# Optimization experiments

Measured on AMD Instinct MI355X. Metric: run time of the kernel, lower is better.

## Reference

```python
import jax, jax.numpy as jnp
import numpy as np

DIM = 3456      # visual_dim
E = 1024        # embed_dim = dim_head*heads = 128*8
H = 8
D = E // H
LN_EPS = 1e-5


def _mlp(x, w1, b1, w2, b2):
    # nn.Sequential(Linear, GELU(exact), Linear)
    h = jax.nn.gelu(x @ w1.T + b1, approximate=False)
    return h @ w2.T + b2


def _ln(x, g, b):
    m = jnp.mean(x, axis=-1, keepdims=True)
    v = jnp.mean((x - m) ** 2, axis=-1, keepdims=True)
    return (x - m) * jax.lax.rsqrt(v + LN_EPS) * g + b


def setup_inputs() -> dict:
    key = jax.random.key(0)
    ks = jax.random.split(key, 24)
    std = 0.02
    d = {"x": jax.random.normal(ks[0], (5, 729, DIM), dtype=jnp.float32)}
    i = 1
    for name in ("q", "k", "v"):
        d[f"{name}_w1"] = std * jax.random.normal(ks[i], (E, DIM), dtype=jnp.float32); i += 1
        d[f"{name}_b1"] = jnp.zeros((E,), jnp.float32)
        d[f"{name}_w2"] = std * jax.random.normal(ks[i], (E, E), dtype=jnp.float32); i += 1
        d[f"{name}_b2"] = jnp.zeros((E,), jnp.float32)
        d[f"ln_{name}_g"] = jnp.ones((E,), jnp.float32)
        d[f"ln_{name}_b"] = jnp.zeros((E,), jnp.float32)
    d["in_proj_w"] = std * jax.random.normal(ks[i], (3 * E, E), dtype=jnp.float32); i += 1
    d["in_proj_b"] = jnp.zeros((3 * E,), jnp.float32)
    d["out_proj_w"] = std * jax.random.normal(ks[i], (E, E), dtype=jnp.float32); i += 1
    d["out_proj_b"] = jnp.zeros((E,), jnp.float32)
    d["to_out_w"] = std * jax.random.normal(ks[i], (DIM, E), dtype=jnp.float32)
    return d


def reference(x,
              q_w1, q_b1, q_w2, q_b2, ln_q_g, ln_q_b,
              k_w1, k_b1, k_w2, k_b2, ln_k_g, ln_k_b,
              v_w1, v_b1, v_w2, v_b2, ln_v_g, ln_v_b,
              in_proj_w, in_proj_b, out_proj_w, out_proj_b, to_out_w):
    t, hw, c = x.shape
    # spatial_temporal pattern: x_multi = x, no interpolation.
    # q/k/v: MLP -> LN -> permute(1,0,2) -> divide_feature -> flatten.
    # divide_feature is a pure permutation of tokens; all tokens end up in a
    # single (L, 1, E) attention, so full attention over the flattened
    # (hw, t) token order computes the identical result.
    q = _ln(_mlp(x, q_w1, q_b1, q_w2, q_b2), ln_q_g, ln_q_b)  # (t, hw, E)
    k = _ln(_mlp(x, k_w1, k_b1, k_w2, k_b2), ln_k_g, ln_k_b)
    v = _ln(_mlp(x, v_w1, v_b1, v_w2, v_b2), ln_v_g, ln_v_b)
    L = t * hw
    q = q.transpose(1, 0, 2).reshape(L, E)  # (hw*t, E), (h,w,t)-major order
    k = k.transpose(1, 0, 2).reshape(L, E)
    v = v.transpose(1, 0, 2).reshape(L, E)
    # nn.MultiheadAttention with packed in_proj
    qp = (q @ in_proj_w[:E].T + in_proj_b[:E]).reshape(L, H, D)
    kp = (k @ in_proj_w[E:2 * E].T + in_proj_b[E:2 * E]).reshape(L, H, D)
    vp = (v @ in_proj_w[2 * E:].T + in_proj_b[2 * E:]).reshape(L, H, D)
    scale = 1.0 / jnp.sqrt(jnp.asarray(D, q.dtype))
    scores = jnp.einsum('qhd,khd->hqk', qp, kp) * scale  # (H, L, L)
    attn = jax.nn.softmax(scores, axis=-1)
    o = jnp.einsum('hqk,khd->qhd', attn, vp).reshape(L, E)
    o = o @ out_proj_w.T + out_proj_b
    o = o.reshape(hw, t, E).transpose(1, 0, 2)  # (t, hw, E)
    out = o @ to_out_w.T                         # (t, hw, c)
    return x + out
```

## Files before the change

kernel.cpp:

```cpp
#include <hip/hip_runtime.h>
#include <hip/hip_bf16.h>

#define L_TOK 3645
#define MP    3712
#define DIMV  3456
#define EDIM  1024

typedef __attribute__((ext_vector_type(8))) short bf8;
typedef __attribute__((ext_vector_type(4))) short s4v;
typedef __attribute__((ext_vector_type(4))) float f4;

__device__ __forceinline__ short f2b(float f) {
  union { float f; unsigned u; } v; v.f = f;
  unsigned r = v.u + 0x7fffu + ((v.u >> 16) & 1u);
  return (short)(r >> 16);
}
__device__ __forceinline__ float b2f(short s) {
  union { unsigned u; float f; } v; v.u = ((unsigned)(unsigned short)s) << 16;
  return v.f;
}
__device__ __forceinline__ void gld16(const void* g, void* l) {
  __builtin_amdgcn_global_load_lds(
      (const __attribute__((address_space(1))) void*)(unsigned long long)g,
      (__attribute__((address_space(3))) void*)(unsigned)(unsigned long long)l,
      16, 0, 0);
}

__global__ __launch_bounds__(256) void k_cvt(const float* __restrict__ src,
                                             short* __restrict__ dst, int n4) {
  int i = blockIdx.x * 256 + threadIdx.x;
  if (i >= n4) return;
  float4 v = ((const float4*)src)[i];
  s4v o; o[0] = f2b(v.x); o[1] = f2b(v.y); o[2] = f2b(v.z); o[3] = f2b(v.w);
  ((s4v*)dst)[i] = o;
}
__global__ __launch_bounds__(256) void k_cvt_pad(const float* __restrict__ src,
                                                 short* __restrict__ dst, int n4src, int n4tot) {
  int i = blockIdx.x * 256 + threadIdx.x;
  if (i >= n4tot) return;
  s4v o; o[0] = 0; o[1] = 0; o[2] = 0; o[3] = 0;
  if (i < n4src) {
    float4 v = ((const float4*)src)[i];
    o[0] = f2b(v.x); o[1] = f2b(v.y); o[2] = f2b(v.z); o[3] = f2b(v.w);
  }
  ((s4v*)dst)[i] = o;
}

#define GM_GELU   0
#define GM_BIAS   1
#define GM_QSCALE 2
#define GM_RESID  3

template<int MODE>
__global__ __launch_bounds__(256)
void k_gemm(const short* __restrict__ A, long sA,
            const short* __restrict__ B, long sB,
            const float* __restrict__ bias0, const float* __restrict__ bias1,
            const float* __restrict__ bias2,
            void* __restrict__ Cout, long sC,
            int N, int K, const float* __restrict__ resid)
{
  __shared__ short As[3][128 * 32];
  __shared__ short Bs[3][128 * 32];
  const int tid  = threadIdx.x;
  const int z    = blockIdx.z;

  const int nwg  = gridDim.x * gridDim.y;
  const int orig = blockIdx.y * gridDim.x + blockIdx.x;
  const int qq   = nwg >> 3, rr = nwg & 7;
  const int xcd  = orig & 7, ofs = orig >> 3;
  const int swz  = (xcd < rr ? xcd * (qq + 1) : rr * (qq + 1) + (xcd - rr) * qq) + ofs;
  const int brow = (swz / gridDim.x) * 128;
  const int bcol = (swz % gridDim.x) * 128;

  const short* Ab = A + (long)z * sA;
  const short* Bb = B + (long)z * sB;
  const float* bias = (z == 0) ? bias0 : (z == 1 ? bias1 : bias2);

  const int wave = tid >> 6, lane = tid & 63;
  const int lg = lane >> 4, lc = lane & 15;
  const int m0 = (wave >> 1) * 64, n0 = (wave & 1) * 64;

  const int r0 = tid >> 2, seg = tid & 3;
  const int r1 = r0 + 64;
  const int so0 = (seg ^ ((r0 >> 1) & 3)) * 8;
  const int so1 = (seg ^ ((r1 >> 1) & 3)) * 8;
  const short* pA0 = Ab + (long)(brow + r0) * K + so0;
  const short* pA1 = Ab + (long)(brow + r1) * K + so1;
  const short* pB0 = Bb + (long)(bcol + r0) * K + so0;
  const short* pB1 = Bb + (long)(bcol + r1) * K + so1;

  f4 acc[4][4];
  f4 zero = {0.f, 0.f, 0.f, 0.f};
#pragma unroll
  for (int i = 0; i < 4; ++i)
#pragma unroll
    for (int j = 0; j < 4; ++j) acc[i][j] = zero;

  auto STAGE = [&](int buf) {
    gld16(pA0, &As[buf][tid * 8]);
    gld16(pA1, &As[buf][(tid + 256) * 8]);
    gld16(pB0, &Bs[buf][tid * 8]);
    gld16(pB1, &Bs[buf][(tid + 256) * 8]);
    pA0 += 32; pA1 += 32; pB0 += 32; pB1 += 32;
  };

  const int NT = K >> 5;
  STAGE(0);
  STAGE(1);

  for (int t = 0; t < NT; ++t) {
    const int buf = t % 3;
    if (t < NT - 1) { asm volatile("s_waitcnt vmcnt(4)" ::: "memory"); }
    else           { asm volatile("s_waitcnt vmcnt(0)" ::: "memory"); }
    __builtin_amdgcn_sched_barrier(0);
    __builtin_amdgcn_s_barrier();
    if (t + 2 < NT) STAGE((t + 2) % 3);

    const short* Al = &As[buf][0];
    const short* Bl = &Bs[buf][0];
    bf8 af[4], bfr[4];
#pragma unroll
    for (int mi = 0; mi < 4; ++mi) {
      int r = m0 + mi * 16 + lc;
      af[mi] = *(const bf8*)&Al[r * 32 + ((lg ^ ((r >> 1) & 3)) * 8)];
    }
#pragma unroll
    for (int ni = 0; ni < 4; ++ni) {
      int r = n0 + ni * 16 + lc;
      bfr[ni] = *(const bf8*)&Bl[r * 32 + ((lg ^ ((r >> 1) & 3)) * 8)];
    }
#pragma unroll
    for (int mi = 0; mi < 4; ++mi)
#pragma unroll
      for (int ni = 0; ni < 4; ++ni)
        acc[mi][ni] = __builtin_amdgcn_mfma_f32_16x16x32_bf16(af[mi], bfr[ni], acc[mi][ni], 0, 0, 0);
    __builtin_amdgcn_sched_barrier(0);
  }

  if (MODE == GM_RESID) {
    float* C = (float*)Cout;
#pragma unroll
    for (int ni = 0; ni < 4; ++ni) {
      int col = bcol + n0 + ni * 16 + lc;
#pragma unroll
      for (int mi = 0; mi < 4; ++mi)
#pragma unroll
        for (int r = 0; r < 4; ++r) {
          int row = brow + m0 + mi * 16 + lg * 4 + r;
          if (row < L_TOK)
            C[(long)row * N + col] = acc[mi][ni][r] + resid[(long)row * N + col];
        }
    }
  } else {
    short* C = (short*)Cout + (long)z * sC;
    const float alpha = (MODE == GM_QSCALE && z == 0) ? 0.08838834764831845f : 1.0f;
#pragma unroll
    for (int ni = 0; ni < 4; ++ni) {
      int col = bcol + n0 + ni * 16 + lc;
      float bv = bias[col];
#pragma unroll
      for (int mi = 0; mi < 4; ++mi)
#pragma unroll
        for (int r = 0; r < 4; ++r) {
          int row = brow + m0 + mi * 16 + lg * 4 + r;
          float v = acc[mi][ni][r] + bv;
          if (MODE == GM_GELU) v = 0.5f * v * (1.f + erff(v * 0.70710678118654752f));
          v *= alpha;
          C[(long)row * EDIM + col] = f2b(v);
        }
    }
  }
}

__global__ __launch_bounds__(256)
void k_ln(const short* __restrict__ A, short* __restrict__ Y,
          const float* __restrict__ g0, const float* __restrict__ g1, const float* __restrict__ g2,
          const float* __restrict__ b0, const float* __restrict__ b1, const float* __restrict__ b2)
{
  const int row = blockIdx.x, z = blockIdx.y;
  const float* g = (z == 0) ? g0 : (z == 1 ? g1 : g2);
  const float* b = (z == 0) ? b0 : (z == 1 ? b1 : b2);
  const short* a = A + ((long)z * MP + row) * EDIM;
  short* y = Y + ((long)z * MP + row) * EDIM;
  const int t = threadIdx.x;
  s4v v = *(const s4v*)&a[t * 4];
  float x0 = b2f(v[0]), x1 = b2f(v[1]), x2 = b2f(v[2]), x3 = b2f(v[3]);
  float s = x0 + x1 + x2 + x3;
  float q = x0 * x0 + x1 * x1 + x2 * x2 + x3 * x3;
#pragma unroll
  for (int off = 1; off < 64; off <<= 1) { s += __shfl_xor(s, off); q += __shfl_xor(q, off); }
  __shared__ float rs[4], rq[4];
  if ((t & 63) == 0) { rs[t >> 6] = s; rq[t >> 6] = q; }
  __syncthreads();
  s = rs[0] + rs[1] + rs[2] + rs[3];
  q = rq[0] + rq[1] + rq[2] + rq[3];
  float mean = s * (1.f / 1024.f);
  float var  = q * (1.f / 1024.f) - mean * mean;
  float rstd = rsqrtf(var + 1e-5f);
  s4v o;
#pragma unroll
  for (int j = 0; j < 4; ++j) {
    int col = t * 4 + j;
    o[j] = f2b((b2f(v[j]) - mean) * rstd * g[col] + b[col]);
  }
  *(s4v*)&y[t * 4] = o;
}

__global__ __launch_bounds__(256)
void k_vtrans(const short* __restrict__ vp, short* __restrict__ vpT)
{
  const int kb = blockIdx.x * 64, h = blockIdx.y;
  __shared__ short T[64 * 128];
  const int tid = threadIdx.x;
#pragma unroll
  for (int i = 0; i < 4; ++i) {
    int c = tid + 256 * i;
    int r = c >> 4, x = c & 15;
    bf8 val = *(const bf8*)&vp[(long)(kb + r) * EDIM + h * 128 + x * 8];
    *(bf8*)&T[r * 128 + ((x ^ (r & 7)) * 8)] = val;
  }
  __syncthreads();
#pragma unroll
  for (int i = 0; i < 4; ++i) {
    int c = tid + 256 * i;
    int dr = c >> 3, x = c & 7;
    short tmp[8];
#pragma unroll
    for (int e = 0; e < 8; ++e) {
      int kv = x * 8 + e;
      tmp[e] = T[kv * 128 + (((dr >> 3) ^ (kv & 7)) << 3) + (dr & 7)];
    }
    *(bf8*)&vpT[((long)h * 128 + dr) * MP + kb + x * 8] = *(bf8*)tmp;
  }
}

__global__ __launch_bounds__(256)
void k_attn(const short* __restrict__ qp, const short* __restrict__ kp,
            const short* __restrict__ vpT, short* __restrict__ o)
{
  const int bx = blockIdx.x;
  const int h = bx & 7, qb = (bx >> 3) * 64;
  const int tid = threadIdx.x, wave = tid >> 6, lane = tid & 63;
  const int lg = lane >> 4, lc = lane & 15;
  __shared__ short Ks[64 * 128];
  __shared__ short Vs[128 * 64];
  __shared__ short Ps[4][16 * 64];

  const int qrow = qb + wave * 16 + lc;
  bf8 qf[4];
#pragma unroll
  for (int d4 = 0; d4 < 4; ++d4)
    qf[d4] = *(const bf8*)&qp[(long)qrow * EDIM + h * 128 + d4 * 32 + lg * 8];

  f4 oacc[8];
  f4 zero = {0.f, 0.f, 0.f, 0.f};
#pragma unroll
  for (int dt = 0; dt < 8; ++dt) oacc[dt] = zero;
  float lsum = 0.f;

  for (int kb = 0; kb < L_TOK; kb += 64) {
#pragma unroll
    for (int i = 0; i < 4; ++i) {
      int c = tid + 256 * i; int r = c >> 4, x = c & 15;
      gld16(&kp[(long)(kb + r) * EDIM + h * 128 + (x ^ (r & 7)) * 8], &Ks[c * 8]);
    }
#pragma unroll
    for (int i = 0; i < 4; ++i) {
      int c = tid + 256 * i; int dr = c >> 3, x = c & 7;
      gld16(&vpT[((long)h * 128 + dr) * MP + kb + (x ^ (dr & 7)) * 8], &Vs[c * 8]);
    }
    __syncthreads();

#pragma unroll
    for (int s = 0; s < 4; ++s) {
      f4 sa = zero;
      const int krow = s * 16 + lc;
#pragma unroll
      for (int d4 = 0; d4 < 4; ++d4) {
        bf8 kf = *(const bf8*)&Ks[krow * 128 + (((d4 * 4 + lg) ^ (krow & 7)) * 8)];
        sa = __builtin_amdgcn_mfma_f32_16x16x32_bf16(kf, qf[d4], sa, 0, 0, 0);
      }
      const int kvb = kb + s * 16 + lg * 4;
      float p[4];
#pragma unroll
      for (int r = 0; r < 4; ++r) {
        float e = __expf(sa[r]);
        p[r] = (kvb + r < L_TOK) ? e : 0.f;
        lsum += p[r];
      }
      s4v pk; pk[0] = f2b(p[0]); pk[1] = f2b(p[1]); pk[2] = f2b(p[2]); pk[3] = f2b(p[3]);
      *(s4v*)&Ps[wave][lc * 64 + ((s * 16 + lg * 4) ^ ((lc & 7) << 3))] = pk;
    }
    bf8 pf0 = *(const bf8*)&Ps[wave][lc * 64 + ((lg * 8) ^ ((lc & 7) << 3))];
    bf8 pf1 = *(const bf8*)&Ps[wave][lc * 64 + ((32 + lg * 8) ^ ((lc & 7) << 3))];
#pragma unroll
    for (int dt = 0; dt < 8; ++dt) {
      const int vrow = dt * 16 + lc;
      bf8 vf0 = *(const bf8*)&Vs[vrow * 64 + ((lg ^ (vrow & 7)) * 8)];
      bf8 vf1 = *(const bf8*)&Vs[vrow * 64 + (((4 + lg) ^ (vrow & 7)) * 8)];
      oacc[dt] = __builtin_amdgcn_mfma_f32_16x16x32_bf16(pf0, vf0, oacc[dt], 0, 0, 0);
      oacc[dt] = __builtin_amdgcn_mfma_f32_16x16x32_bf16(pf1, vf1, oacc[dt], 0, 0, 0);
    }
    __syncthreads();
  }

  lsum += __shfl_xor(lsum, 16);
  lsum += __shfl_xor(lsum, 32);
  float rinv[4];
#pragma unroll
  for (int r = 0; r < 4; ++r) rinv[r] = 1.f / __shfl(lsum, lg * 4 + r);
#pragma unroll
  for (int dt = 0; dt < 8; ++dt)
#pragma unroll
    for (int r = 0; r < 4; ++r) {
      int orow = qb + wave * 16 + lg * 4 + r;
      o[(long)orow * EDIM + h * 128 + dt * 16 + lc] = f2b(oacc[dt][r] * rinv[r]);
    }
}

extern "C" void kernel_launch(void* const* d_in, const int* in_sizes, int n_in,
                              void* d_out, int out_size, void* d_ws, size_t ws_size,
                              hipStream_t stream)
{
  const float* x   = (const float*)d_in[0];
  const float* ipb = (const float*)d_in[20];
  const float* opb = (const float*)d_in[22];

  char* ws = (char*)d_ws;
  short* regA = (short*)(ws + 0);
  short* regB = (short*)(ws + 25657344);
  short* w1b  = (short*)(ws + 48463872);
  short* w2b  = (short*)(ws + 69697536);
  short* wpb  = (short*)(ws + 75988992);
  short* wob  = (short*)(ws + 82280448);
  short* wtb  = (short*)(ws + 84377600);
  short* vpT  = (short*)(ws + 91455488);

  short* xb  = regA;
  short* h1  = regB;
  short* aln = regA;
  short* lnq = regB;
  short* proj = regA;
  short* ob  = regB;
  short* o2  = (short*)(ws + 25657344 + 7602176);

  k_cvt_pad<<<12528, 256, 0, stream>>>(x, xb, 3149280, 3207168);
  k_cvt<<<3456, 256, 0, stream>>>((const float*)d_in[1],  w1b,            884736);
  k_cvt<<<3456, 256, 0, stream>>>((const float*)d_in[7],  w1b + 3538944,  884736);
  k_cvt<<<3456, 256, 0, stream>>>((const float*)d_in[13], w1b + 7077888,  884736);
  k_cvt<<<1024, 256, 0, stream>>>((const float*)d_in[3],  w2b,            262144);
  k_cvt<<<1024, 256, 0, stream>>>((const float*)d_in[9],  w2b + 1048576,  262144);
  k_cvt<<<1024, 256, 0, stream>>>((const float*)d_in[15], w2b + 2097152,  262144);
  k_cvt<<<3072, 256, 0, stream>>>((const float*)d_in[19], wpb,            786432);
  k_cvt<<<1024, 256, 0, stream>>>((const float*)d_in[21], wob,            262144);
  k_cvt<<<3456, 256, 0, stream>>>((const float*)d_in[23], wtb,            884736);

  dim3 g3(8, 29, 3), g1(8, 29, 1);
  k_gemm<GM_GELU><<<g3, 256, 0, stream>>>(xb, 0, w1b, 3538944,
      (const float*)d_in[2], (const float*)d_in[8], (const float*)d_in[14],
      h1, (long)MP * EDIM, EDIM, DIMV, nullptr);
  k_gemm<GM_BIAS><<<g3, 256, 0, stream>>>(h1, (long)MP * EDIM, w2b, 1048576,
      (const float*)d_in[4], (const float*)d_in[10], (const float*)d_in[16],
      aln, (long)MP * EDIM, EDIM, EDIM, nullptr);
  dim3 gl(MP, 3);
  k_ln<<<gl, 256, 0, stream>>>(aln, lnq,
      (const float*)d_in[5], (const float*)d_in[11], (const float*)d_in[17],
      (const float*)d_in[6], (const float*)d_in[12], (const float*)d_in[18]);
  k_gemm<GM_QSCALE><<<g3, 256, 0, stream>>>(lnq, (long)MP * EDIM, wpb, 1048576,
      ipb, ipb + 1024, ipb + 2048,
      proj, (long)MP * EDIM, EDIM, EDIM, nullptr);
  dim3 gt(MP / 64, 8);
  k_vtrans<<<gt, 256, 0, stream>>>(proj + 2L * MP * EDIM, vpT);
  k_attn<<<(MP / 64) * 8, 256, 0, stream>>>(proj, proj + (long)MP * EDIM, vpT, ob);
  k_gemm<GM_BIAS><<<g1, 256, 0, stream>>>(ob, 0, wob, 0,
      opb, opb, opb, o2, 0, EDIM, EDIM, nullptr);
  dim3 g5(27, 29, 1);
  k_gemm<GM_RESID><<<g5, 256, 0, stream>>>(o2, 0, wtb, 0,
      nullptr, nullptr, nullptr, d_out, 0, DIMV, EDIM, x);
}
```

Baseline: 444.7 us.

## Double-buffer K/V tiles in attention and raise MFMA wave priority

```diff
diff --git a/kernel.cpp b/kernel.cpp
--- a/kernel.cpp
+++ b/kernel.cpp
@@ -130,11 +130,13 @@
       int r = n0 + ni * 16 + lc;
       bfr[ni] = *(const bf8*)&Bl[r * 32 + ((lg ^ ((r >> 1) & 3)) * 8)];
     }
+    __builtin_amdgcn_s_setprio(1);
 #pragma unroll
     for (int mi = 0; mi < 4; ++mi)
 #pragma unroll
       for (int ni = 0; ni < 4; ++ni)
         acc[mi][ni] = __builtin_amdgcn_mfma_f32_16x16x32_bf16(af[mi], bfr[ni], acc[mi][ni], 0, 0, 0);
+    __builtin_amdgcn_s_setprio(0);
     __builtin_amdgcn_sched_barrier(0);
   }
 
@@ -243,8 +245,8 @@
   const int h = bx & 7, qb = (bx >> 3) * 64;
   const int tid = threadIdx.x, wave = tid >> 6, lane = tid & 63;
   const int lg = lane >> 4, lc = lane & 15;
-  __shared__ short Ks[64 * 128];
-  __shared__ short Vs[128 * 64];
+  __shared__ short Ks[2][64 * 128];
+  __shared__ short Vs[2][128 * 64];
   __shared__ short Ps[4][16 * 64];
 
   const int qrow = qb + wave * 16 + lc;
@@ -259,28 +261,50 @@
   for (int dt = 0; dt < 8; ++dt) oacc[dt] = zero;
   float lsum = 0.f;
 
-  for (int kb = 0; kb < L_TOK; kb += 64) {
+  auto STAGE = [&](short* ksb, short* vsb, int kb) {
 #pragma unroll
     for (int i = 0; i < 4; ++i) {
       int c = tid + 256 * i; int r = c >> 4, x = c & 15;
-      gld16(&kp[(long)(kb + r) * EDIM + h * 128 + (x ^ (r & 7)) * 8], &Ks[c * 8]);
+      gld16(&kp[(long)(kb + r) * EDIM + h * 128 + (x ^ (r & 7)) * 8], &ksb[c * 8]);
     }
 #pragma unroll
     for (int i = 0; i < 4; ++i) {
       int c = tid + 256 * i; int dr = c >> 3, x = c & 7;
-      gld16(&vpT[((long)h * 128 + dr) * MP + kb + (x ^ (dr & 7)) * 8], &Vs[c * 8]);
-    }
-    __syncthreads();
+      gld16(&vpT[((long)h * 128 + dr) * MP + kb + (x ^ (dr & 7)) * 8], &vsb[c * 8]);
+    }
+  };
+
+  const int NTILE = (L_TOK + 63) / 64;
+  STAGE(Ks[0], Vs[0], 0);
+
+  for (int t = 0; t < NTILE; ++t) {
+    const int kb = t * 64;
+    const short* ksb = Ks[t & 1];
+    const short* vsb = Vs[t & 1];
+    __builtin_amdgcn_s_barrier();
+    if (t + 1 < NTILE) {
+      STAGE(Ks[(t + 1) & 1], Vs[(t + 1) & 1], kb + 64);
+      asm volatile("s_waitcnt vmcnt(8)" ::: "memory");
+    } else {
+      asm volatile("s_waitcnt vmcnt(0)" ::: "memory");
+    }
+    __builtin_amdgcn_sched_barrier(0);
+    __builtin_amdgcn_s_barrier();
+    __builtin_amdgcn_sched_barrier(0);
 
 #pragma unroll
     for (int s = 0; s < 4; ++s) {
       f4 sa = zero;
       const int krow = s * 16 + lc;
-#pragma unroll
-      for (int d4 = 0; d4 < 4; ++d4) {
-        bf8 kf = *(const bf8*)&Ks[krow * 128 + (((d4 * 4 + lg) ^ (krow & 7)) * 8)];
-        sa = __builtin_amdgcn_mfma_f32_16x16x32_bf16(kf, qf[d4], sa, 0, 0, 0);
-      }
+      bf8 kf[4];
+#pragma unroll
+      for (int d4 = 0; d4 < 4; ++d4)
+        kf[d4] = *(const bf8*)&ksb[krow * 128 + (((d4 * 4 + lg) ^ (krow & 7)) * 8)];
+      __builtin_amdgcn_s_setprio(1);
+#pragma unroll
+      for (int d4 = 0; d4 < 4; ++d4)
+        sa = __builtin_amdgcn_mfma_f32_16x16x32_bf16(kf[d4], qf[d4], sa, 0, 0, 0);
+      __builtin_amdgcn_s_setprio(0);
       const int kvb = kb + s * 16 + lg * 4;
       float p[4];
 #pragma unroll
@@ -297,12 +321,14 @@
 #pragma unroll
     for (int dt = 0; dt < 8; ++dt) {
       const int vrow = dt * 16 + lc;
-      bf8 vf0 = *(const bf8*)&Vs[vrow * 64 + ((lg ^ (vrow & 7)) * 8)];
-      bf8 vf1 = *(const bf8*)&Vs[vrow * 64 + (((4 + lg) ^ (vrow & 7)) * 8)];
+      bf8 vf0 = *(const bf8*)&vsb[vrow * 64 + ((lg ^ (vrow & 7)) * 8)];
+      bf8 vf1 = *(const bf8*)&vsb[vrow * 64 + (((4 + lg) ^ (vrow & 7)) * 8)];
+      __builtin_amdgcn_s_setprio(1);
       oacc[dt] = __builtin_amdgcn_mfma_f32_16x16x32_bf16(pf0, vf0, oacc[dt], 0, 0, 0);
       oacc[dt] = __builtin_amdgcn_mfma_f32_16x16x32_bf16(pf1, vf1, oacc[dt], 0, 0, 0);
-    }
-    __syncthreads();
+      __builtin_amdgcn_s_setprio(0);
+    }
+    __builtin_amdgcn_sched_barrier(0);
   }
 
   lsum += __shfl_xor(lsum, 16);
```

After: 417.8 us. -6.0%, faster.
